# Performance work log

Measured on AMD Instinct MI355X. Metric: run time of the kernel, lower is better.

Reference implementation:

```python
import jax, jax.numpy as jnp
import numpy as np

B, T, L, V, C = 4096, 200, 8, 64, 16
N_BERN = 32        # first 32 vars are bernoulli (sigmoid link), last 32 poisson (exp link)
LINPRED_MAX = 20.0


def setup_inputs() -> dict:
    key = jax.random.key(0)
    ks = jax.random.split(key, 6)
    return {
        "epsilon": jax.random.normal(ks[0], (B, T, L), dtype=jnp.float32),
        "u": jax.random.normal(ks[1], (B, 1, V), dtype=jnp.float32),
        "x": jax.random.normal(ks[2], (B, T, C), dtype=jnp.float32),
        # learned parameters (per VARGLLVM.__init__)
        "A": jax.random.normal(ks[3], (L, L), dtype=jnp.float32) * 0.1,
        "logvar_z1": jnp.zeros((L,), dtype=jnp.float32),
        "beta0": jnp.zeros((L,), dtype=jnp.float32),   # VAR1_intercept (frozen zeros)
        "beta1": jnp.zeros((L,), dtype=jnp.float32),   # VAR1_slope (frozen zeros)
        "intercepts": jnp.zeros((V,), dtype=jnp.float32),
        "wz": jax.random.normal(ks[4], (L, V), dtype=jnp.float32) * 0.1,
        "wx": jax.random.normal(ks[5], (C, V), dtype=jnp.float32) * 0.1,
        "logvar_u": jnp.zeros((V,), dtype=jnp.float32),
    }


def _var1(epsilon, A, logvar_z1, beta0, beta1):
    """z_1 = eps_1 * sqrt(exp(logvar_z1)); z_t = z_{t-1} @ A + beta0 + beta1*t + eps_t."""
    z0 = epsilon[:, 0, :] * jnp.exp(0.5 * logvar_z1)          # (B, L)
    eps_rest = jnp.swapaxes(epsilon[:, 1:, :], 0, 1)          # (T-1, B, L)
    ts = jnp.arange(1, epsilon.shape[1], dtype=epsilon.dtype)  # (T-1,)

    def step(z_prev, inp):
        eps_t, t = inp
        z_t = z_prev @ A + beta0 + beta1 * t + eps_t
        return z_t, z_t

    _, zs = jax.lax.scan(step, z0, (eps_rest, ts))            # (T-1, B, L)
    z = jnp.concatenate([z0[None], zs], axis=0)               # (T, B, L)
    return jnp.swapaxes(z, 0, 1)                              # (B, T, L)


def reference(epsilon, u, x, A, logvar_z1, beta0, beta1, intercepts, wz, wx, logvar_u):
    z = _var1(epsilon, A, logvar_z1, beta0, beta1)            # (B, T, L)
    linpar = (intercepts[None, None, :]
              + x @ wx                                        # (B, T, V)
              + z @ wz                                        # (B, T, V)
              + u * jnp.exp(0.5 * logvar_u)[None, None, :])   # broadcast (B, 1, V)
    linpar = jnp.clip(linpar, -LINPRED_MAX, LINPRED_MAX)
    is_bern = jnp.arange(V) < N_BERN                          # (V,) link selector
    condmean = jnp.where(is_bern, jax.nn.sigmoid(linpar), jnp.exp(linpar))
    return linpar, condmean
```

## Files before the change

### kernel.cpp

```cpp
#include <hip/hip_runtime.h>
#include <hip/hip_bf16.h>

#define BB 4096
#define TT 200
#define LL 8
#define VV 64
#define CC 16
#define NBERN 32
#define CLIP 20.0f
#define TC 25
#define NCH (TT / TC)
#define TOTW (BB * NCH)
#define WPB 4
#define LBLK (TOTW / WPB)
#define XF4 (TC * CC / 4)
#define ZF4 (TC * LL / 4)
#define BUF4T (XF4 + ZF4)

__global__ __launch_bounds__(256) void var1_fast(
    const float* __restrict__ eps,
    const float* __restrict__ A,
    const float* __restrict__ logvar_z1,
    const float* __restrict__ beta0,
    const float* __restrict__ beta1,
    float* __restrict__ zout)
{
    const int tid  = blockIdx.x * 256 + threadIdx.x;
    const int b    = tid >> 3;
    const int j    = tid & 7;
    const int lane = threadIdx.x & 63;
    const int gbase = lane & 56;

    float Acol[LL];
#pragma unroll
    for (int l = 0; l < LL; ++l) Acol[l] = A[l * LL + j];
    const float bb0 = beta0[j];
    const float bb1 = beta1[j];
    const float s1  = __expf(0.5f * logvar_z1[j]);

    const float* ep = eps + (size_t)b * TT * LL + j;
    float* zb = zout + (size_t)b * TT * LL + j;

    float zj = ep[0] * s1;
    zb[0] = zj;

    float ebuf[4];
#pragma unroll
    for (int k = 0; k < 4; ++k) ebuf[k] = ep[(size_t)(1 + k) * LL];

#pragma unroll 4
    for (int t = 1; t < TT; ++t) {
        const int slot = (t - 1) & 3;
        const float cur = ebuf[slot];
        const int tn = t + 4;
        if (tn < TT) ebuf[slot] = ep[(size_t)tn * LL];

        float a = fmaf(bb1, (float)t, bb0) + cur;
#pragma unroll
        for (int l = 0; l < LL; ++l) {
            const float zl = __shfl(zj, gbase + l);
            a = fmaf(zl, Acol[l], a);
        }
        zj = a;
        zb[(size_t)t * LL] = zj;
    }
}

__global__ __launch_bounds__(256) void link_nt(
    const float* __restrict__ z,
    const float* __restrict__ u,
    const float* __restrict__ x,
    const float* __restrict__ intercepts,
    const float* __restrict__ wz,
    const float* __restrict__ wx,
    const float* __restrict__ logvar_u,
    float* __restrict__ lp_out,
    float* __restrict__ cm_out)
{
    const int w    = threadIdx.x >> 6;
    const int lane = threadIdx.x & 63;
    const int gw   = blockIdx.x * WPB + w;
    const int b    = gw >> 3;
    const int t0   = (gw & 7) * TC;
    const int v    = lane;

    __shared__ __align__(16) float4 buf[WPB][BUF4T];

    float wxv[CC];
#pragma unroll
    for (int c = 0; c < CC; ++c) wxv[c] = wx[c * VV + v];
    float wzv[LL];
#pragma unroll
    for (int l = 0; l < LL; ++l) wzv[l] = wz[l * VV + v];
    const float base = intercepts[v] + u[(size_t)b * VV + v] * __expf(0.5f * logvar_u[v]);

    const float4* gx4 = (const float4*)(x + ((size_t)b * TT + t0) * CC);
    const float4* gz4 = (const float4*)(z + ((size_t)b * TT + t0) * LL);
    float4* bw = buf[w];
    {
        const int i0 = lane;
        bw[i0] = (i0 < XF4) ? gx4[i0] : gz4[i0 - XF4];
        const int i1 = lane + 64;
        bw[i1] = (i1 < XF4) ? gx4[i1] : gz4[i1 - XF4];
        const int i2 = lane + 128;
        if (i2 < BUF4T) bw[i2] = gz4[i2 - XF4];
    }

    const float4* xs4 = bw;
    const float4* zs4 = bw + XF4;

    float* lp = lp_out + ((size_t)b * TT + t0) * VV + v;
    float* cm = cm_out + ((size_t)b * TT + t0) * VV + v;

    float4 cx0 = xs4[0], cx1 = xs4[1], cx2 = xs4[2], cx3 = xs4[3];
    float4 cz0 = zs4[0], cz1 = zs4[1];

    for (int tt = 0; tt < TC; ++tt) {
        float4 nx0, nx1, nx2, nx3, nz0, nz1;
        if (tt + 1 < TC) {
            nx0 = xs4[(tt + 1) * 4 + 0]; nx1 = xs4[(tt + 1) * 4 + 1];
            nx2 = xs4[(tt + 1) * 4 + 2]; nx3 = xs4[(tt + 1) * 4 + 3];
            nz0 = zs4[(tt + 1) * 2 + 0]; nz1 = zs4[(tt + 1) * 2 + 1];
        }

        float a0 = base, a1 = 0.f, a2 = 0.f, a3 = 0.f;
        a0 = fmaf(cx0.x, wxv[0],  a0); a0 = fmaf(cx0.y, wxv[1],  a0);
        a0 = fmaf(cx0.z, wxv[2],  a0); a0 = fmaf(cx0.w, wxv[3],  a0);
        a1 = fmaf(cx1.x, wxv[4],  a1); a1 = fmaf(cx1.y, wxv[5],  a1);
        a1 = fmaf(cx1.z, wxv[6],  a1); a1 = fmaf(cx1.w, wxv[7],  a1);
        a2 = fmaf(cx2.x, wxv[8],  a2); a2 = fmaf(cx2.y, wxv[9],  a2);
        a2 = fmaf(cx2.z, wxv[10], a2); a2 = fmaf(cx2.w, wxv[11], a2);
        a3 = fmaf(cx3.x, wxv[12], a3); a3 = fmaf(cx3.y, wxv[13], a3);
        a3 = fmaf(cx3.z, wxv[14], a3); a3 = fmaf(cx3.w, wxv[15], a3);
        a0 = fmaf(cz0.x, wzv[0],  a0); a0 = fmaf(cz0.y, wzv[1],  a0);
        a1 = fmaf(cz0.z, wzv[2],  a1); a1 = fmaf(cz0.w, wzv[3],  a1);
        a2 = fmaf(cz1.x, wzv[4],  a2); a2 = fmaf(cz1.y, wzv[5],  a2);
        a3 = fmaf(cz1.z, wzv[6],  a3); a3 = fmaf(cz1.w, wzv[7],  a3);

        float acc = (a0 + a1) + (a2 + a3);
        acc = fminf(fmaxf(acc, -CLIP), CLIP);
        const float cmv = (v < NBERN) ? (1.0f / (1.0f + __expf(-acc)))
                                      : __expf(acc);
        __builtin_nontemporal_store(acc, lp + (size_t)tt * VV);
        __builtin_nontemporal_store(cmv, cm + (size_t)tt * VV);

        cx0 = nx0; cx1 = nx1; cx2 = nx2; cx3 = nx3;
        cz0 = nz0; cz1 = nz1;
    }
}

__global__ __launch_bounds__(256) void vargllvm_fused(
    const float* __restrict__ eps, const float* __restrict__ u,
    const float* __restrict__ x, const float* __restrict__ A,
    const float* __restrict__ logvar_z1, const float* __restrict__ beta0,
    const float* __restrict__ beta1, const float* __restrict__ intercepts,
    const float* __restrict__ wz, const float* __restrict__ wx,
    const float* __restrict__ logvar_u,
    float* __restrict__ linpar_out, float* __restrict__ condmean_out)
{
    const int wave = threadIdx.x >> 6;
    const int lane = threadIdx.x & 63;
    const int b    = blockIdx.x * 4 + wave;
    const int v    = lane;

    float wxv[CC];
#pragma unroll
    for (int c = 0; c < CC; ++c) wxv[c] = wx[c * VV + v];
    float wzv[LL];
#pragma unroll
    for (int l = 0; l < LL; ++l) wzv[l] = wz[l * VV + v];
    const float base = intercepts[v] + u[(size_t)b * VV + v] * __expf(0.5f * logvar_u[v]);

    float Ar[LL][LL];
#pragma unroll
    for (int l = 0; l < LL; ++l)
#pragma unroll
        for (int j = 0; j < LL; ++j) Ar[l][j] = A[l * LL + j];
    float b0[LL], b1[LL];
#pragma unroll
    for (int j = 0; j < LL; ++j) { b0[j] = beta0[j]; b1[j] = beta1[j]; }

    const float* epsb = eps + (size_t)b * TT * LL;
    const float* xb   = x   + (size_t)b * TT * CC;
    float* lp = linpar_out   + (size_t)b * TT * VV + v;
    float* cm = condmean_out + (size_t)b * TT * VV + v;

    float zv[LL];
#pragma unroll
    for (int j = 0; j < LL; ++j) zv[j] = epsb[j] * __expf(0.5f * logvar_z1[j]);

    for (int t = 0; t < TT; ++t) {
        if (t > 0) {
            float zn[LL];
            const float tf = (float)t;
#pragma unroll
            for (int j = 0; j < LL; ++j) {
                float a = fmaf(b1[j], tf, b0[j]) + epsb[t * LL + j];
#pragma unroll
                for (int l = 0; l < LL; ++l) a = fmaf(zv[l], Ar[l][j], a);
                zn[j] = a;
            }
#pragma unroll
            for (int j = 0; j < LL; ++j) zv[j] = zn[j];
        }
        float acc = base;
#pragma unroll
        for (int c = 0; c < CC; ++c) acc = fmaf(xb[t * CC + c], wxv[c], acc);
#pragma unroll
        for (int l = 0; l < LL; ++l) acc = fmaf(zv[l], wzv[l], acc);
        acc = fminf(fmaxf(acc, -CLIP), CLIP);
        float cmv = (v < NBERN) ? (1.0f / (1.0f + __expf(-acc))) : __expf(acc);
        lp[(size_t)t * VV] = acc;
        cm[(size_t)t * VV] = cmv;
    }
}

extern "C" void kernel_launch(void* const* d_in, const int* in_sizes, int n_in,
                              void* d_out, int out_size, void* d_ws, size_t ws_size,
                              hipStream_t stream) {
    const float* eps        = (const float*)d_in[0];
    const float* u          = (const float*)d_in[1];
    const float* x          = (const float*)d_in[2];
    const float* A          = (const float*)d_in[3];
    const float* logvar_z1  = (const float*)d_in[4];
    const float* beta0      = (const float*)d_in[5];
    const float* beta1      = (const float*)d_in[6];
    const float* intercepts = (const float*)d_in[7];
    const float* wz         = (const float*)d_in[8];
    const float* wx         = (const float*)d_in[9];
    const float* logvar_u   = (const float*)d_in[10];

    float* linpar   = (float*)d_out;
    float* condmean = (float*)d_out + (size_t)BB * TT * VV;

    const size_t z_bytes = (size_t)BB * TT * LL * sizeof(float);
    if (ws_size >= z_bytes) {
        float* zws = (float*)d_ws;
        hipLaunchKernelGGL(var1_fast, dim3(BB * LL / 256), dim3(256), 0, stream,
                           eps, A, logvar_z1, beta0, beta1, zws);
        hipLaunchKernelGGL(link_nt, dim3(LBLK), dim3(256), 0, stream,
                           zws, u, x, intercepts, wz, wx, logvar_u, linpar, condmean);
    } else {
        hipLaunchKernelGGL(vargllvm_fused, dim3(BB / 4), dim3(256), 0, stream,
                           eps, u, x, A, logvar_z1, beta0, beta1,
                           intercepts, wz, wx, logvar_u, linpar, condmean);
    }
}
```

Before: 106.9 us.

## Parallelize VAR(1) recurrence over time segments with A^25 carry propagation

Replaces the serial per-batch VAR(1) scan with a segmented parallel scan. Each of 8 threads per batch handles a 25-step time segment, the segment boundary states are combined using a precomputed A^25 matrix, and then each segment is recomputed from its corrected initial state. Eps is staged through shared memory with float4 loads. This shortens the serial dependency chain from 200 steps to about 25+7+25. The cost is roughly doubled arithmetic, a 51KB shared buffer that limits occupancy, and a small floating-point reassociation difference.

New measurement: 114.2 us. 1.07x slower.

```diff
diff --git a/kernel.cpp b/kernel.cpp
--- a/kernel.cpp
+++ b/kernel.cpp
@@ -16,8 +16,9 @@
 #define XF4 (TC * CC / 4)
 #define ZF4 (TC * LL / 4)
 #define BUF4T (XF4 + ZF4)
-
-__global__ __launch_bounds__(256) void var1_fast(
+#define SEGT 25
+
+__global__ __launch_bounds__(64) void var1_v3(
     const float* __restrict__ eps,
     const float* __restrict__ A,
     const float* __restrict__ logvar_z1,
@@ -25,44 +26,145 @@
     const float* __restrict__ beta1,
     float* __restrict__ zout)
 {
-    const int tid  = blockIdx.x * 256 + threadIdx.x;
-    const int b    = tid >> 3;
-    const int j    = tid & 7;
-    const int lane = threadIdx.x & 63;
-    const int gbase = lane & 56;
-
-    float Acol[LL];
-#pragma unroll
-    for (int l = 0; l < LL; ++l) Acol[l] = A[l * LL + j];
-    const float bb0 = beta0[j];
-    const float bb1 = beta1[j];
-    const float s1  = __expf(0.5f * logvar_z1[j]);
-
-    const float* ep = eps + (size_t)b * TT * LL + j;
-    float* zb = zout + (size_t)b * TT * LL + j;
-
-    float zj = ep[0] * s1;
-    zb[0] = zj;
-
-    float ebuf[4];
-#pragma unroll
-    for (int k = 0; k < 4; ++k) ebuf[k] = ep[(size_t)(1 + k) * LL];
-
-#pragma unroll 4
-    for (int t = 1; t < TT; ++t) {
-        const int slot = (t - 1) & 3;
-        const float cur = ebuf[slot];
-        const int tn = t + 4;
-        if (tn < TT) ebuf[slot] = ep[(size_t)tn * LL];
-
-        float a = fmaf(bb1, (float)t, bb0) + cur;
-#pragma unroll
-        for (int l = 0; l < LL; ++l) {
-            const float zl = __shfl(zj, gbase + l);
-            a = fmaf(zl, Acol[l], a);
-        }
-        zj = a;
-        zb[(size_t)t * LL] = zj;
+    const int tid = threadIdx.x;
+    const int bl  = tid >> 3;
+    const int s   = tid & 7;
+    const int b   = blockIdx.x * 8 + bl;
+
+    __shared__ __align__(16) float epsS[8 * TT * LL];
+    __shared__ float Mb[2][64];
+    __shared__ float Pw8[64];
+    __shared__ float P[64];
+    __shared__ float zendS[8][8][8];
+    __shared__ float initS[8][8][8];
+
+    {
+        const float4* src = (const float4*)(eps + (size_t)blockIdx.x * 8 * TT * LL);
+        float4* dst = (float4*)epsS;
+        for (int i = tid; i < 8 * TT * LL / 4; i += 64) dst[i] = src[i];
+    }
+
+    const int pi = tid >> 3, pj = tid & 7;
+    Mb[0][tid] = A[pi * 8 + pj];
+    __syncthreads();
+    float v;
+    v = 0.f;
+#pragma unroll
+    for (int l = 0; l < 8; ++l) v = fmaf(Mb[0][pi*8+l], Mb[0][l*8+pj], v);
+    Mb[1][tid] = v; __syncthreads();
+    v = 0.f;
+#pragma unroll
+    for (int l = 0; l < 8; ++l) v = fmaf(Mb[1][pi*8+l], Mb[1][l*8+pj], v);
+    Mb[0][tid] = v; __syncthreads();
+    v = 0.f;
+#pragma unroll
+    for (int l = 0; l < 8; ++l) v = fmaf(Mb[0][pi*8+l], Mb[0][l*8+pj], v);
+    Mb[1][tid] = v; Pw8[tid] = v; __syncthreads();
+    v = 0.f;
+#pragma unroll
+    for (int l = 0; l < 8; ++l) v = fmaf(Mb[1][pi*8+l], Mb[1][l*8+pj], v);
+    Mb[0][tid] = v; __syncthreads();
+    v = 0.f;
+#pragma unroll
+    for (int l = 0; l < 8; ++l) v = fmaf(Mb[0][pi*8+l], Pw8[l*8+pj], v);
+    Mb[1][tid] = v; __syncthreads();
+    v = 0.f;
+#pragma unroll
+    for (int l = 0; l < 8; ++l) v = fmaf(Mb[1][pi*8+l], A[l*8+pj], v);
+    P[tid] = v; __syncthreads();
+
+    float Am[8][8], B0[8], B1[8], SL[8];
+#pragma unroll
+    for (int l = 0; l < 8; ++l)
+#pragma unroll
+        for (int jj = 0; jj < 8; ++jj) Am[l][jj] = A[l * 8 + jj];
+#pragma unroll
+    for (int jj = 0; jj < 8; ++jj) {
+        B0[jj] = beta0[jj];
+        B1[jj] = beta1[jj];
+        SL[jj] = __expf(0.5f * logvar_z1[jj]);
+    }
+
+    const float* myeps = epsS + ((bl * TT) + s * SEGT) * LL;
+    const int k0 = (s == 0) ? 1 : 0;
+
+    float z[8];
+#pragma unroll
+    for (int jj = 0; jj < 8; ++jj) z[jj] = 0.f;
+    if (s == 0) {
+#pragma unroll
+        for (int jj = 0; jj < 8; ++jj) z[jj] = myeps[jj] * SL[jj];
+    }
+    for (int k = k0; k < SEGT; ++k) {
+        const int t = s * SEGT + k;
+        const float4 e0 = *(const float4*)(myeps + k * 8);
+        const float4 e1 = *(const float4*)(myeps + k * 8 + 4);
+        const float ef[8] = {e0.x, e0.y, e0.z, e0.w, e1.x, e1.y, e1.z, e1.w};
+        const float tf = (float)t;
+        float zn[8];
+#pragma unroll
+        for (int jj = 0; jj < 8; ++jj) {
+            float a = fmaf(B1[jj], tf, B0[jj]) + ef[jj];
+#pragma unroll
+            for (int l = 0; l < 8; ++l) a = fmaf(z[l], Am[l][jj], a);
+            zn[jj] = a;
+        }
+#pragma unroll
+        for (int jj = 0; jj < 8; ++jj) z[jj] = zn[jj];
+    }
+#pragma unroll
+    for (int jj = 0; jj < 8; ++jj) zendS[bl][s][jj] = z[jj];
+    __syncthreads();
+
+    if (s == 0) {
+        float E[8];
+#pragma unroll
+        for (int jj = 0; jj < 8; ++jj) E[jj] = zendS[bl][0][jj];
+        for (int ss = 1; ss < 8; ++ss) {
+#pragma unroll
+            for (int jj = 0; jj < 8; ++jj) initS[bl][ss][jj] = E[jj];
+            float En[8];
+#pragma unroll
+            for (int jj = 0; jj < 8; ++jj) {
+                float c = 0.f;
+#pragma unroll
+                for (int l = 0; l < 8; ++l) c = fmaf(E[l], P[l * 8 + jj], c);
+                En[jj] = zendS[bl][ss][jj] + c;
+            }
+#pragma unroll
+            for (int jj = 0; jj < 8; ++jj) E[jj] = En[jj];
+        }
+    }
+    __syncthreads();
+
+    float* zb = zout + ((size_t)b * TT + s * SEGT) * LL;
+    if (s == 0) {
+#pragma unroll
+        for (int jj = 0; jj < 8; ++jj) z[jj] = myeps[jj] * SL[jj];
+        *(float4*)(zb)     = make_float4(z[0], z[1], z[2], z[3]);
+        *(float4*)(zb + 4) = make_float4(z[4], z[5], z[6], z[7]);
+    } else {
+#pragma unroll
+        for (int jj = 0; jj < 8; ++jj) z[jj] = initS[bl][s][jj];
+    }
+    for (int k = k0; k < SEGT; ++k) {
+        const int t = s * SEGT + k;
+        const float4 e0 = *(const float4*)(myeps + k * 8);
+        const float4 e1 = *(const float4*)(myeps + k * 8 + 4);
+        const float ef[8] = {e0.x, e0.y, e0.z, e0.w, e1.x, e1.y, e1.z, e1.w};
+        const float tf = (float)t;
+        float zn[8];
+#pragma unroll
+        for (int jj = 0; jj < 8; ++jj) {
+            float a = fmaf(B1[jj], tf, B0[jj]) + ef[jj];
+#pragma unroll
+            for (int l = 0; l < 8; ++l) a = fmaf(z[l], Am[l][jj], a);
+            zn[jj] = a;
+        }
+#pragma unroll
+        for (int jj = 0; jj < 8; ++jj) z[jj] = zn[jj];
+        *(float4*)(zb + (size_t)k * 8)     = make_float4(z[0], z[1], z[2], z[3]);
+        *(float4*)(zb + (size_t)k * 8 + 4) = make_float4(z[4], z[5], z[6], z[7]);
     }
 }
 
@@ -236,7 +338,7 @@
     const size_t z_bytes = (size_t)BB * TT * LL * sizeof(float);
     if (ws_size >= z_bytes) {
         float* zws = (float*)d_ws;
-        hipLaunchKernelGGL(var1_fast, dim3(BB * LL / 256), dim3(256), 0, stream,
+        hipLaunchKernelGGL(var1_v3, dim3(BB / 8), dim3(64), 0, stream,
                            eps, A, logvar_z1, beta0, beta1, zws);
         hipLaunchKernelGGL(link_nt, dim3(LBLK), dim3(256), 0, stream,
                            zws, u, x, intercepts, wz, wx, logvar_u, linpar, condmean);
```
